# Kernel optimization log

Measured on AMD Instinct MI355X. Metric: run time of the kernel, lower is better.

## Reference

```python
import jax, jax.numpy as jnp
import numpy as np
from jax import lax

ALPHA = 0.95
THETA = 1.0
GAMMA = 12.0
GAIN = 1.0  # gain buffer value used in forward (detached in torch via .item())
KERNELS = (8, 16, 32)
B, T = 256, 16384


@jax.custom_vjp
def surrogate_spike(x):
    # forward: hard threshold at 0
    return (x >= 0).astype(x.dtype)


def _spike_fwd(x):
    return surrogate_spike(x), x


def _spike_bwd(x, g):
    ax = jnp.abs(GAMMA * x)
    grad = (ax < 1.0).astype(x.dtype) * (1.0 - ax) * GAMMA
    return (g * grad,)


surrogate_spike.defvjp(_spike_fwd, _spike_bwd)


def causal_conv(x, w):
    # x: [B,1,T], w: [1,1,k] -> [B,T]; left-pad k-1 (causal), cross-correlation like torch Conv1d
    k = w.shape[-1]
    out = lax.conv_general_dilated(
        x, w, window_strides=(1,), padding=[(k - 1, 0)],
        dimension_numbers=("NCH", "OIH", "NCH"))
    return out[:, 0, :]


def lif_wta(u):
    # u: [B,K,T] -> spikes s_all [B,K,T]
    Bb, K, Tt = u.shape

    def step(v, u_t):  # v,u_t: [B,K]
        v = ALPHA * v + u_t
        m = v - THETA
        s_raw = surrogate_spike(m)
        mask = jax.nn.one_hot(jnp.argmax(m, axis=1), K, dtype=m.dtype)  # top-1 WTA
        s = s_raw * mask
        return v - s * THETA, s

    v0 = jnp.zeros((Bb, K), u.dtype)
    _, s_all = lax.scan(step, v0, jnp.moveaxis(u, 2, 0))  # [T,B,K]
    return jnp.moveaxis(s_all, 0, 2)  # [B,K,T]


def setup_inputs() -> dict:
    key = jax.random.key(0)
    kx, k0, k1, k2, ky = jax.random.split(key, 5)
    x = jax.random.normal(kx, (B, 1, T), dtype=jnp.float32)
    w0 = jax.random.normal(k0, (1, 1, 8), dtype=jnp.float32) / np.sqrt(8.0)
    w1 = jax.random.normal(k1, (1, 1, 16), dtype=jnp.float32) / np.sqrt(16.0)
    w2 = jax.random.normal(k2, (1, 1, 32), dtype=jnp.float32) / np.sqrt(32.0)
    y = jax.random.randint(ky, (B, T), 0, 2, dtype=jnp.int32)
    return {"x": x, "w0": w0, "w1": w1, "w2": w2, "y": y}


def reference(x, w0, w1, w2, y):
    ws = (w0, w1, w2)
    # per-branch causal conv, scaled by 1/sqrt(k), then gain
    u = jnp.stack(
        [causal_conv(x, w) * (1.0 / np.sqrt(float(k))) for w, k in zip(ws, KERNELS)],
        axis=1) * GAIN  # [B,K,T]
    s_all = lif_wta(u)
    return (u, s_all)
```

## Files before the change

### kernel.cpp

```cpp
#include <hip/hip_runtime.h>
#include <math.h>

constexpr int B = 256;
constexpr int T = 16384;
constexpr int K = 3;

constexpr int CHUNK = 128;
constexpr int WARM  = 512;

constexpr int CBT = 128;
constexpr int CWT = 32;


__global__ __launch_bounds__(256, 2) void conv_kernel(
    const float* __restrict__ x,
    const float* __restrict__ w0f,
    const float* __restrict__ w1f,
    const float* __restrict__ w2f,
    float*  __restrict__ u_out,
    float*  __restrict__ w32)
{
    const int blk = blockIdx.x;
    const int bgi = blk >> 7;
    const int t0  = (blk & 127) * CBT;
    const int b0  = bgi * 64;
    const int tid = threadIdx.x;

    __shared__ float sx[64][164];
    for (int k = tid; k < 64 * 40; k += 256) {
        const int r  = k / 40;
        const int c4 = k - r * 40;
        const int g  = t0 - 32 + 4 * c4;
        float4 v = make_float4(0.f, 0.f, 0.f, 0.f);
        if (g >= 0) v = *(const float4*)(x + (size_t)(b0 + r) * T + g);
        *(float4*)&sx[r][4 * c4] = v;
    }
    __syncthreads();

    const int lane    = tid & 63;
    const int w       = tid >> 6;
    const int t_start = t0 + CWT * w;

    double w0d[8], w1d[16], w2d[32];
#pragma unroll
    for (int i = 0; i < 8; ++i)  w0d[i] = (double)w0f[i];
#pragma unroll
    for (int i = 0; i < 16; ++i) w1d[i] = (double)w1f[i];
#pragma unroll
    for (int i = 0; i < 32; ++i) w2d[i] = (double)w2f[i];

    double win[32];
#pragma unroll
    for (int k = 1; k < 32; ++k) win[k] = (double)sx[lane][CWT * w + k];

    const double s8  = 1.0 / sqrt(8.0);
    const double s32 = 1.0 / sqrt(32.0);

    float fr0[16], fr1[16], fr2[16];
    float4 pf;
    float* uf = u_out + (size_t)(b0 + lane) * (3 * T);

#define PPUT(v, D) do {                                                       \
    const float _pv = (v);                                                    \
    if (((D) & 3) == 0) pf.x = _pv;                                           \
    else if (((D) & 3) == 1) pf.y = _pv;                                      \
    else if (((D) & 3) == 2) pf.z = _pv;                                      \
    else {                                                                    \
        pf.w = _pv;                                                           \
        *(float4*)(wq + ((D) >> 2) * 256) = pf;                               \
    }                                                                         \
} while (0)

#pragma unroll
    for (int j = 0; j < CWT; ++j) {
        win[j & 31] = (double)sx[lane][CWT * w + 32 + j];
        double a0 = 0.0, a1 = 0.0, a2 = 0.0;
#pragma unroll
        for (int i = 0; i < 8; ++i)  a0 = fma(w0d[i], win[(j + 25 + i) & 31], a0);
#pragma unroll
        for (int i = 0; i < 16; ++i) a1 = fma(w1d[i], win[(j + 17 + i) & 31], a1);
#pragma unroll
        for (int i = 0; i < 32; ++i) a2 = fma(w2d[i], win[(j + 1 + i) & 31], a2);
        a0 *= s8; a1 *= 0.25; a2 *= s32;

        const int t = t_start + j;
        float* wq = w32 + ((size_t)(t >> 4) * 4 + bgi) * 3072 + lane * 4;
        const int D0 = (j & 15) * 3;
        PPUT((float)(a0 - 0.05), D0);
        PPUT((float)(a1 - 0.05), D0 + 1);
        PPUT((float)(a2 - 0.05), D0 + 2);

        fr0[j & 15] = (float)a0; fr1[j & 15] = (float)a1; fr2[j & 15] = (float)a2;
        if ((j & 15) == 15) {
            float* d = uf + t_start + (j & ~15);
#pragma unroll
            for (int q = 0; q < 4; ++q) {
                *(float4*)(d + 4 * q)         = ((float4*)fr0)[q];
                *(float4*)(d + T + 4 * q)     = ((float4*)fr1)[q];
                *(float4*)(d + 2 * T + 4 * q) = ((float4*)fr2)[q];
            }
        }
    }
#undef PPUT
}

__global__ __launch_bounds__(64, 1) void scan_kernel(
    const float* __restrict__ w32,
    float* __restrict__ s_out)
{
    const int phys = blockIdx.x;
    const int xcd  = phys & 7;
    const int slot = phys >> 3;
    const int c    = xcd * 16 + (slot & 15);
    const int bg   = slot >> 4;
    const int lane = threadIdx.x;

    const int t_emit = c * CHUNK;
    const int t_w    = (t_emit >= WARM) ? (t_emit - WARM) : 0;
    const int warm_g = (t_emit - t_w) >> 4;
    const int n_g    = warm_g + (CHUNK >> 4);
    const int tw16   = t_w >> 4;

    __shared__ float4 lbuf[3 * 768];
    __shared__ float4 sstage[12 * 65];

    double m0 = -1.0, m1 = -1.0, m2 = -1.0;

#define WAITN(N) do {                                                   \
    asm volatile("s_waitcnt vmcnt(" #N ")" ::: "memory");               \
    __builtin_amdgcn_sched_barrier(0);                                  \
} while (0)

#define LOADDMA(s, gg) do {                                                   \
    const float4* _src = (const float4*)(w32 +                                \
        ((size_t)(tw16 + (gg)) * 4 + bg) * 3072) + lane;                      \
    _Pragma("unroll")                                                         \
    for (int _q = 0; _q < 12; ++_q)                                           \
        __builtin_amdgcn_global_load_lds(                                     \
            (const __attribute__((address_space(1))) void*)(const void*)      \
                (_src + (size_t)_q * 64),                                     \
            (__attribute__((address_space(3))) void*)(void*)                  \
                (&lbuf[(s) * 768 + _q * 64]),                                 \
            16, 0, 0);                                                        \
} while (0)

#define STEP(W0, W1, W2, O0, O1, O2) do {                               \
    const double M0 = fma(0.95, m0, (W0));                              \
    const double M1 = fma(0.95, m1, (W1));                              \
    const double M2 = fma(0.95, m2, (W2));                              \
    const bool c01 = (M0 >= M1);                                        \
    const bool c02 = (M0 >= M2);                                        \
    const bool c12 = (M1 >= M2);                                        \
    const bool f0  = (M0 >= 0.0);                                       \
    const bool f1  = (M1 >= 0.0);                                       \
    const bool f2  = (M2 >= 0.0);                                       \
    const bool s0 = c01 & c02 & f0;             \
    const bool s1 = (!c01) & c12 & f1;                                  \
    const bool s2 = (!c02) & (!c12) & f2;                               \
    m0 = s0 ? M0 - 1.0 : M0;                                            \
    m1 = s1 ? M1 - 1.0 : M1;                                            \
    m2 = s2 ? M2 - 1.0 : M2;                                            \
    (O0) = s0 ? 1.0f : 0.0f;                                            \
    (O1) = s1 ? 1.0f : 0.0f;                                            \
    (O2) = s2 ? 1.0f : 0.0f;                                            \
} while (0)

#define GETW(d) ( ((d) & 3) == 0 ? _rf[(d) >> 2].x                      \
                : ((d) & 3) == 1 ? _rf[(d) >> 2].y                      \
                : ((d) & 3) == 2 ? _rf[(d) >> 2].z                      \
                :                  _rf[(d) >> 2].w )

#define BODY(s, pp) do {                                                      \
    if ((pp) < n_g) {                                                         \
        if ((pp) == n_g - 1)            WAITN(36);                            \
        else if ((pp) == n_g - 2)       WAITN(48);                            \
        else if ((pp) >= warm_g + 3)    WAITN(60);                            \
        else if ((pp) == warm_g + 2)    WAITN(48);                            \
        else if ((pp) == warm_g + 1)    WAITN(36);                            \
        else                            WAITN(24);                            \
        const float4* _lp = lbuf + (s) * 768 + lane;                          \
        float4 _rf[12];                                                       \
        _Pragma("unroll")                                                     \
        for (int _q = 0; _q < 12; ++_q) _rf[_q] = _lp[(size_t)_q * 64];       \
        float sp0[16], sp1[16], sp2[16];                                      \
        _Pragma("unroll")                                                     \
        for (int _j = 0; _j < 16; ++_j) {                                     \
            const int _d0 = 3 * _j;                                           \
            const double _W0 = (double)GETW(_d0);                             \
            const double _W1 = (double)GETW(_d0 + 1);                         \
            const double _W2 = (double)GETW(_d0 + 2);                         \
            STEP(_W0, _W1, _W2, sp0[_j], sp1[_j], sp2[_j]);                   \
        }                                                                     \
        if ((pp) + 3 < n_g) LOADDMA(s, (pp) + 3);                             \
        if ((pp) >= warm_g) {                                                 \
            _Pragma("unroll")                                                 \
            for (int _q = 0; _q < 4; ++_q) {                                  \
                sstage[(0 * 4 + _q) * 65 + lane] = ((float4*)sp0)[_q];        \
                sstage[(1 * 4 + _q) * 65 + lane] = ((float4*)sp1)[_q];        \
                sstage[(2 * 4 + _q) * 65 + lane] = ((float4*)sp2)[_q];        \
            }                                                                 \
            asm volatile("s_waitcnt lgkmcnt(0)" ::: "memory");                \
            __builtin_amdgcn_sched_barrier(0);                                \
            const int _t = t_w + (pp) * 16;                                   \
            _Pragma("unroll")                                                 \
            for (int _k = 0; _k < 3; ++_k) {                                  \
                _Pragma("unroll")                                             \
                for (int _g = 0; _g < 4; ++_g) {                              \
                    const float4 _v =                                         \
                        sstage[(_k * 4 + (lane & 3)) * 65 + _g * 16 + (lane >> 2)]; \
                    float* _dst = s_out                                       \
                        + (size_t)(bg * 64 + _g * 16 + (lane >> 2)) * (3 * T) \
                        + (size_t)_k * T + _t + (lane & 3) * 4;               \
                    *(float4*)_dst = _v;                                      \
                }                                                             \
            }                                                                 \
        }                                                                     \
    }                                                                         \
} while (0)

    LOADDMA(0, 0);
    LOADDMA(1, 1);
    LOADDMA(2, 2);
    for (int p = 0; p < 48; p += 3) {
        if (p >= n_g) break;
        BODY(0, p);
        BODY(1, p + 1);
        BODY(2, p + 2);
    }

#undef BODY
#undef GETW
#undef STEP
#undef LOADDMA
#undef WAITN
}

extern "C" void kernel_launch(void* const* d_in, const int* in_sizes, int n_in,
                              void* d_out, int out_size, void* d_ws, size_t ws_size,
                              hipStream_t stream)
{
    const float* x  = (const float*)d_in[0];
    const float* w0 = (const float*)d_in[1];
    const float* w1 = (const float*)d_in[2];
    const float* w2 = (const float*)d_in[3];

    float* out   = (float*)d_out;
    float* u_out = out;
    float* s_out = out + (size_t)B * K * T;

    float* w32 = (float*)d_ws;

    conv_kernel<<<(B / 64) * (T / CBT), 256, 0, stream>>>(x, w0, w1, w2, u_out, w32);
    scan_kernel<<<(B / 64) * (T / CHUNK), 64, 0, stream>>>(w32, s_out);
}
```

Baseline: 208.0 us.

## Fuse conv and scan kernels with per-tile readiness flags

```diff
diff --git a/kernel.cpp b/kernel.cpp
--- a/kernel.cpp
+++ b/kernel.cpp
@@ -12,53 +12,62 @@
 constexpr int CWT = 32;
 
 
-__global__ __launch_bounds__(256, 2) void conv_kernel(
+__global__ __launch_bounds__(256, 2) void fused_kernel(
     const float* __restrict__ x,
     const float* __restrict__ w0f,
     const float* __restrict__ w1f,
     const float* __restrict__ w2f,
-    float*  __restrict__ u_out,
-    float*  __restrict__ w32)
+    float* __restrict__ u_out,
+    float* __restrict__ s_out,
+    float* __restrict__ w32,
+    unsigned* __restrict__ flags)
 {
-    const int blk = blockIdx.x;
-    const int bgi = blk >> 7;
-    const int t0  = (blk & 127) * CBT;
-    const int b0  = bgi * 64;
+    __shared__ union SH {
+        struct { float sx[64][164]; } c;
+        struct { float4 lbuf[3 * 768]; float4 sstage[12 * 65]; } s;
+    } sh;
+
     const int tid = threadIdx.x;
-
-    __shared__ float sx[64][164];
-    for (int k = tid; k < 64 * 40; k += 256) {
-        const int r  = k / 40;
-        const int c4 = k - r * 40;
-        const int g  = t0 - 32 + 4 * c4;
-        float4 v = make_float4(0.f, 0.f, 0.f, 0.f);
-        if (g >= 0) v = *(const float4*)(x + (size_t)(b0 + r) * T + g);
-        *(float4*)&sx[r][4 * c4] = v;
-    }
-    __syncthreads();
-
-    const int lane    = tid & 63;
-    const int w       = tid >> 6;
-    const int t_start = t0 + CWT * w;
-
-    double w0d[8], w1d[16], w2d[32];
-#pragma unroll
-    for (int i = 0; i < 8; ++i)  w0d[i] = (double)w0f[i];
-#pragma unroll
-    for (int i = 0; i < 16; ++i) w1d[i] = (double)w1f[i];
-#pragma unroll
-    for (int i = 0; i < 32; ++i) w2d[i] = (double)w2f[i];
-
-    double win[32];
-#pragma unroll
-    for (int k = 1; k < 32; ++k) win[k] = (double)sx[lane][CWT * w + k];
-
-    const double s8  = 1.0 / sqrt(8.0);
-    const double s32 = 1.0 / sqrt(32.0);
-
-    float fr0[16], fr1[16], fr2[16];
-    float4 pf;
-    float* uf = u_out + (size_t)(b0 + lane) * (3 * T);
+    const int bid = blockIdx.x;
+
+    if (bid < 512) {
+        const int blk = bid;
+        const int bgi = blk >> 7;
+        const int t0  = (blk & 127) * CBT;
+        const int b0  = bgi * 64;
+
+        for (int k = tid; k < 64 * 40; k += 256) {
+            const int r  = k / 40;
+            const int c4 = k - r * 40;
+            const int g  = t0 - 32 + 4 * c4;
+            float4 v = make_float4(0.f, 0.f, 0.f, 0.f);
+            if (g >= 0) v = *(const float4*)(x + (size_t)(b0 + r) * T + g);
+            *(float4*)&sh.c.sx[r][4 * c4] = v;
+        }
+        __syncthreads();
+
+        const int lane    = tid & 63;
+        const int w       = tid >> 6;
+        const int t_start = t0 + CWT * w;
+
+        double w0d[8], w1d[16], w2d[32];
+#pragma unroll
+        for (int i = 0; i < 8; ++i)  w0d[i] = (double)w0f[i];
+#pragma unroll
+        for (int i = 0; i < 16; ++i) w1d[i] = (double)w1f[i];
+#pragma unroll
+        for (int i = 0; i < 32; ++i) w2d[i] = (double)w2f[i];
+
+        double win[32];
+#pragma unroll
+        for (int k = 1; k < 32; ++k) win[k] = (double)sh.c.sx[lane][CWT * w + k];
+
+        const double s8  = 1.0 / sqrt(8.0);
+        const double s32 = 1.0 / sqrt(32.0);
+
+        float fr0[16], fr1[16], fr2[16];
+        float4 pf;
+        float* uf = u_out + (size_t)(b0 + lane) * (3 * T);
 
 #define PPUT(v, D) do {                                                       \
     const float _pv = (v);                                                    \
@@ -72,48 +81,53 @@
 } while (0)
 
 #pragma unroll
-    for (int j = 0; j < CWT; ++j) {
-        win[j & 31] = (double)sx[lane][CWT * w + 32 + j];
-        double a0 = 0.0, a1 = 0.0, a2 = 0.0;
-#pragma unroll
-        for (int i = 0; i < 8; ++i)  a0 = fma(w0d[i], win[(j + 25 + i) & 31], a0);
-#pragma unroll
-        for (int i = 0; i < 16; ++i) a1 = fma(w1d[i], win[(j + 17 + i) & 31], a1);
-#pragma unroll
-        for (int i = 0; i < 32; ++i) a2 = fma(w2d[i], win[(j + 1 + i) & 31], a2);
-        a0 *= s8; a1 *= 0.25; a2 *= s32;
-
-        const int t = t_start + j;
-        float* wq = w32 + ((size_t)(t >> 4) * 4 + bgi) * 3072 + lane * 4;
-        const int D0 = (j & 15) * 3;
-        PPUT((float)(a0 - 0.05), D0);
-        PPUT((float)(a1 - 0.05), D0 + 1);
-        PPUT((float)(a2 - 0.05), D0 + 2);
-
-        fr0[j & 15] = (float)a0; fr1[j & 15] = (float)a1; fr2[j & 15] = (float)a2;
-        if ((j & 15) == 15) {
-            float* d = uf + t_start + (j & ~15);
-#pragma unroll
-            for (int q = 0; q < 4; ++q) {
-                *(float4*)(d + 4 * q)         = ((float4*)fr0)[q];
-                *(float4*)(d + T + 4 * q)     = ((float4*)fr1)[q];
-                *(float4*)(d + 2 * T + 4 * q) = ((float4*)fr2)[q];
+        for (int j = 0; j < CWT; ++j) {
+            win[j & 31] = (double)sh.c.sx[lane][CWT * w + 32 + j];
+            double a0 = 0.0, a1 = 0.0, a2 = 0.0;
+#pragma unroll
+            for (int i = 0; i < 8; ++i)  a0 = fma(w0d[i], win[(j + 25 + i) & 31], a0);
+#pragma unroll
+            for (int i = 0; i < 16; ++i) a1 = fma(w1d[i], win[(j + 17 + i) & 31], a1);
+#pragma unroll
+            for (int i = 0; i < 32; ++i) a2 = fma(w2d[i], win[(j + 1 + i) & 31], a2);
+            a0 *= s8; a1 *= 0.25; a2 *= s32;
+
+            const int t = t_start + j;
+            float* wq = w32 + ((size_t)(t >> 4) * 4 + bgi) * 3072 + lane * 4;
+            const int D0 = (j & 15) * 3;
+            PPUT((float)(a0 - 0.05), D0);
+            PPUT((float)(a1 - 0.05), D0 + 1);
+            PPUT((float)(a2 - 0.05), D0 + 2);
+
+            fr0[j & 15] = (float)a0; fr1[j & 15] = (float)a1; fr2[j & 15] = (float)a2;
+            if ((j & 15) == 15) {
+                float* d = uf + t_start + (j & ~15);
+#pragma unroll
+                for (int q = 0; q < 4; ++q) {
+                    *(float4*)(d + 4 * q)         = ((float4*)fr0)[q];
+                    *(float4*)(d + T + 4 * q)     = ((float4*)fr1)[q];
+                    *(float4*)(d + 2 * T + 4 * q) = ((float4*)fr2)[q];
+                }
             }
         }
+#undef PPUT
+
+        __threadfence();
+        __syncthreads();
+        if (tid == 0)
+            __hip_atomic_store(flags + blk, 1u, __ATOMIC_RELEASE,
+                               __HIP_MEMORY_SCOPE_AGENT);
+        return;
     }
-#undef PPUT
-}
-
-__global__ __launch_bounds__(64, 1) void scan_kernel(
-    const float* __restrict__ w32,
-    float* __restrict__ s_out)
-{
-    const int phys = blockIdx.x;
+
+    if (tid >= 64) return;
+
+    const int phys = bid - 512;
     const int xcd  = phys & 7;
     const int slot = phys >> 3;
     const int c    = xcd * 16 + (slot & 15);
     const int bg   = slot >> 4;
-    const int lane = threadIdx.x;
+    const int lane = tid;
 
     const int t_emit = c * CHUNK;
     const int t_w    = (t_emit >= WARM) ? (t_emit - WARM) : 0;
@@ -121,8 +135,19 @@
     const int n_g    = warm_g + (CHUNK >> 4);
     const int tw16   = t_w >> 4;
 
-    __shared__ float4 lbuf[3 * 768];
-    __shared__ float4 sstage[12 * 65];
+    {
+        const int first_t = tw16 >> 3;
+        const int last_t  = (tw16 + n_g - 1) >> 3;
+        for (int tt = first_t; tt <= last_t; ++tt) {
+            const unsigned* f = flags + bg * 128 + tt;
+            while (__hip_atomic_load(f, __ATOMIC_ACQUIRE,
+                                     __HIP_MEMORY_SCOPE_AGENT) == 0u)
+                __builtin_amdgcn_s_sleep(8);
+        }
+    }
+
+    float4* lbuf   = sh.s.lbuf;
+    float4* sstage = sh.s.sstage;
 
     double m0 = -1.0, m1 = -1.0, m2 = -1.0;
 
@@ -248,8 +273,11 @@
     float* u_out = out;
     float* s_out = out + (size_t)B * K * T;
 
-    float* w32 = (float*)d_ws;
-
-    conv_kernel<<<(B / 64) * (T / CBT), 256, 0, stream>>>(x, w0, w1, w2, u_out, w32);
-    scan_kernel<<<(B / 64) * (T / CHUNK), 64, 0, stream>>>(w32, s_out);
+    float*    w32   = (float*)d_ws;
+    unsigned* flags = (unsigned*)((char*)d_ws + (64u << 20));
+
+    hipMemsetAsync(flags, 0, 512 * sizeof(unsigned), stream);
+
+    fused_kernel<<<1024, 256, 0, stream>>>(
+        x, w0, w1, w2, u_out, s_out, w32, flags);
 }
```

New measurement: 348.6 us. +67.6%, slower.

## Move u output stores from conv kernel into the latency-bound scan kernel

Applied to the files above, without the earlier changes.

```diff
diff --git a/kernel.cpp b/kernel.cpp
--- a/kernel.cpp
+++ b/kernel.cpp
@@ -17,7 +17,6 @@
     const float* __restrict__ w0f,
     const float* __restrict__ w1f,
     const float* __restrict__ w2f,
-    float*  __restrict__ u_out,
     float*  __restrict__ w32)
 {
     const int blk = blockIdx.x;
@@ -56,9 +55,7 @@
     const double s8  = 1.0 / sqrt(8.0);
     const double s32 = 1.0 / sqrt(32.0);
 
-    float fr0[16], fr1[16], fr2[16];
     float4 pf;
-    float* uf = u_out + (size_t)(b0 + lane) * (3 * T);
 
 #define PPUT(v, D) do {                                                       \
     const float _pv = (v);                                                    \
@@ -89,23 +86,13 @@
         PPUT((float)(a0 - 0.05), D0);
         PPUT((float)(a1 - 0.05), D0 + 1);
         PPUT((float)(a2 - 0.05), D0 + 2);
-
-        fr0[j & 15] = (float)a0; fr1[j & 15] = (float)a1; fr2[j & 15] = (float)a2;
-        if ((j & 15) == 15) {
-            float* d = uf + t_start + (j & ~15);
-#pragma unroll
-            for (int q = 0; q < 4; ++q) {
-                *(float4*)(d + 4 * q)         = ((float4*)fr0)[q];
-                *(float4*)(d + T + 4 * q)     = ((float4*)fr1)[q];
-                *(float4*)(d + 2 * T + 4 * q) = ((float4*)fr2)[q];
-            }
-        }
     }
 #undef PPUT
 }
 
 __global__ __launch_bounds__(64, 1) void scan_kernel(
     const float* __restrict__ w32,
+    float* __restrict__ u_out,
     float* __restrict__ s_out)
 {
     const int phys = blockIdx.x;
@@ -170,13 +157,30 @@
                 : ((d) & 3) == 2 ? _rf[(d) >> 2].z                      \
                 :                  _rf[(d) >> 2].w )
 
+#define TSTORE(dstbase, tt) do {                                              \
+    _Pragma("unroll")                                                         \
+    for (int _k = 0; _k < 3; ++_k) {                                          \
+        _Pragma("unroll")                                                     \
+        for (int _g = 0; _g < 4; ++_g) {                                      \
+            const float4 _v =                                                 \
+                sstage[(_k * 4 + (lane & 3)) * 65 + _g * 16 + (lane >> 2)];   \
+            float* _dst = (dstbase)                                           \
+                + (size_t)(bg * 64 + _g * 16 + (lane >> 2)) * (3 * T)         \
+                + (size_t)_k * T + (tt) + (lane & 3) * 4;                     \
+            *(float4*)_dst = _v;                                              \
+        }                                                                     \
+    }                                                                         \
+} while (0)
+
+#define LGKM0 do {                                                      \
+    asm volatile("s_waitcnt lgkmcnt(0)" ::: "memory");                  \
+    __builtin_amdgcn_sched_barrier(0);                                  \
+} while (0)
+
 #define BODY(s, pp) do {                                                      \
     if ((pp) < n_g) {                                                         \
-        if ((pp) == n_g - 1)            WAITN(36);                            \
-        else if ((pp) == n_g - 2)       WAITN(48);                            \
-        else if ((pp) >= warm_g + 3)    WAITN(60);                            \
-        else if ((pp) == warm_g + 2)    WAITN(48);                            \
-        else if ((pp) == warm_g + 1)    WAITN(36);                            \
+        if ((pp) >= warm_g + 2)         WAITN(63);                            \
+        else if ((pp) == warm_g + 1)    WAITN(48);                            \
         else                            WAITN(24);                            \
         const float4* _lp = lbuf + (s) * 768 + lane;                          \
         float4 _rf[12];                                                       \
@@ -193,27 +197,36 @@
         }                                                                     \
         if ((pp) + 3 < n_g) LOADDMA(s, (pp) + 3);                             \
         if ((pp) >= warm_g) {                                                 \
+            const int _t = t_w + (pp) * 16;                                   \
+                       \
             _Pragma("unroll")                                                 \
             for (int _q = 0; _q < 4; ++_q) {                                  \
                 sstage[(0 * 4 + _q) * 65 + lane] = ((float4*)sp0)[_q];        \
                 sstage[(1 * 4 + _q) * 65 + lane] = ((float4*)sp1)[_q];        \
                 sstage[(2 * 4 + _q) * 65 + lane] = ((float4*)sp2)[_q];        \
             }                                                                 \
-            asm volatile("s_waitcnt lgkmcnt(0)" ::: "memory");                \
-            __builtin_amdgcn_sched_barrier(0);                                \
-            const int _t = t_w + (pp) * 16;                                   \
+            LGKM0;                                                            \
+            TSTORE(s_out, _t);                                                \
+            LGKM0;            \
+                \
+                \
+            float fu0[16], fu1[16], fu2[16];                                  \
             _Pragma("unroll")                                                 \
-            for (int _k = 0; _k < 3; ++_k) {                                  \
-                _Pragma("unroll")                                             \
-                for (int _g = 0; _g < 4; ++_g) {                              \
-                    const float4 _v =                                         \
-                        sstage[(_k * 4 + (lane & 3)) * 65 + _g * 16 + (lane >> 2)]; \
-                    float* _dst = s_out                                       \
-                        + (size_t)(bg * 64 + _g * 16 + (lane >> 2)) * (3 * T) \
-                        + (size_t)_k * T + _t + (lane & 3) * 4;               \
-                    *(float4*)_dst = _v;                                      \
-                }                                                             \
+            for (int _j = 0; _j < 16; ++_j) {                                 \
+                const int _d0 = 3 * _j;                                       \
+                fu0[_j] = GETW(_d0)     + 0.05f;                              \
+                fu1[_j] = GETW(_d0 + 1) + 0.05f;                              \
+                fu2[_j] = GETW(_d0 + 2) + 0.05f;                              \
             }                                                                 \
+            _Pragma("unroll")                                                 \
+            for (int _q = 0; _q < 4; ++_q) {                                  \
+                sstage[(0 * 4 + _q) * 65 + lane] = ((float4*)fu0)[_q];        \
+                sstage[(1 * 4 + _q) * 65 + lane] = ((float4*)fu1)[_q];        \
+                sstage[(2 * 4 + _q) * 65 + lane] = ((float4*)fu2)[_q];        \
+            }                                                                 \
+            LGKM0;                                                            \
+            TSTORE(u_out, _t);                                                \
+            LGKM0;               \
         }                                                                     \
     }                                                                         \
 } while (0)
@@ -229,6 +242,8 @@
     }
 
 #undef BODY
+#undef LGKM0
+#undef TSTORE
 #undef GETW
 #undef STEP
 #undef LOADDMA
@@ -250,6 +265,6 @@
 
     float* w32 = (float*)d_ws;
 
-    conv_kernel<<<(B / 64) * (T / CBT), 256, 0, stream>>>(x, w0, w1, w2, u_out, w32);
-    scan_kernel<<<(B / 64) * (T / CHUNK), 64, 0, stream>>>(w32, s_out);
+    conv_kernel<<<(B / 64) * (T / CBT), 256, 0, stream>>>(x, w0, w1, w2, w32);
+    scan_kernel<<<(B / 64) * (T / CHUNK), 64, 0, stream>>>(w32, u_out, s_out);
 }
```

Result: faster. 195.1 us (-6.2%).
